# Kernel optimization log

Hardware: AMD Instinct MI355X
Metric: run time of the kernel (lower is better)

## Reference

```python
import jax, jax.numpy as jnp
import numpy as np

INPUT_DIM = 1024
HIDDEN_DIM = 1024
NUM_HEADS = 16
HEAD_DIM = HIDDEN_DIM // NUM_HEADS


def setup_inputs() -> dict:
    key = jax.random.key(0)
    ks = jax.random.split(key, 11)
    B, S = 2, 2048
    s_in = 1.0 / np.sqrt(INPUT_DIM)
    s_hid = 1.0 / np.sqrt(HIDDEN_DIM)
    return {
        "query": jax.random.normal(ks[0], (B, S, INPUT_DIM), jnp.float32),
        "key": jax.random.normal(ks[1], (B, S, INPUT_DIM), jnp.float32),
        "value": jax.random.normal(ks[2], (B, S, INPUT_DIM), jnp.float32),
        "Wq": jax.random.normal(ks[3], (INPUT_DIM, HIDDEN_DIM), jnp.float32) * s_in,
        "bq": jnp.zeros((HIDDEN_DIM,), jnp.float32),
        "Wk": jax.random.normal(ks[4], (INPUT_DIM, HEAD_DIM), jnp.float32) * s_in,
        "bk": jnp.zeros((HEAD_DIM,), jnp.float32),
        "Wv": jax.random.normal(ks[5], (INPUT_DIM, HEAD_DIM), jnp.float32) * s_in,
        "bv": jnp.zeros((HEAD_DIM,), jnp.float32),
        "Wo": jax.random.normal(ks[6], (HIDDEN_DIM, INPUT_DIM), jnp.float32) * s_hid,
        "bo": jnp.zeros((INPUT_DIM,), jnp.float32),
    }


def reference(query, key, value, Wq, bq, Wk, bk, Wv, bv, Wo, bo):
    B, S, _ = query.shape
    # projections
    q = query @ Wq + bq                       # [B,S,H*D]
    k = key @ Wk + bk                         # [B,S,D]  (single shared head)
    v = value @ Wv + bv                       # [B,S,D]
    q = q.reshape(B, S, NUM_HEADS, HEAD_DIM)  # [B,S,H,D]
    # MQA scores: shared K broadcast over query heads
    scores = jnp.einsum('bqhd,bkd->bhqk', q, k) / np.sqrt(HIDDEN_DIM)
    attn = jax.nn.softmax(scores, axis=-1)    # [B,H,Q,K]
    out = jnp.einsum('bhqk,bkd->bqhd', attn, v)  # [B,Q,H,D]
    out = out.reshape(B, S, HIDDEN_DIM)
    return out @ Wo + bo
```

## Files before the change

kernel.cpp:

```cpp
#include <hip/hip_runtime.h>


typedef unsigned int   u32;
typedef unsigned short u16;
typedef union { float4 v; float f[4]; } f4u;
typedef __attribute__((ext_vector_type(8)))  short frag16;
typedef __attribute__((ext_vector_type(4)))  float f32x4;
typedef __attribute__((ext_vector_type(16))) float f32x16;
typedef union { frag16 v; u32 w[4]; u16 e[8]; } bf8u;

static __device__ __forceinline__ u16 f2bf(float x) {
  union { float f; u32 u; } v; v.f = x;
  u32 r = v.u + 0x7fff + ((v.u >> 16) & 1);
  return (u16)(r >> 16);
}

static __device__ __forceinline__ u32 cvt_pk_bf16(float lo, float hi) {
  u32 r;
  asm("v_cvt_pk_bf16_f32 %0, %1, %2" : "=v"(r) : "v"(lo), "v"(hi));
  return r;
}

static __device__ __forceinline__ void gload_lds16(const u16* g, u16* l) {
  __builtin_amdgcn_global_load_lds(
      (const __attribute__((address_space(1))) u32*)g,
      (__attribute__((address_space(3))) u32*)l, 16, 0, 0);
}

static __device__ void tcvt_tile(const float* __restrict__ src,
                                 u16* __restrict__ dst,
                                 int C, int ldT, int rt, int ct,
                                 float (*t)[65]) {
  const int r0 = rt * 64, c0 = ct * 64;
  const int tr  = threadIdx.x >> 4;
  const int tc4 = (threadIdx.x & 15) * 4;
#pragma unroll
  for (int i = 0; i < 4; ++i) {
    f4u v; v.v = *(const float4*)(src + (size_t)(r0 + tr + i * 16) * C + c0 + tc4);
    t[tr + i * 16][tc4 + 0] = v.f[0];
    t[tr + i * 16][tc4 + 1] = v.f[1];
    t[tr + i * 16][tc4 + 2] = v.f[2];
    t[tr + i * 16][tc4 + 3] = v.f[3];
  }
  __syncthreads();
#pragma unroll
  for (int i = 0; i < 4; ++i) {
    const int oc = tr + i * 16;
    ushort4 o;
    o.x = f2bf(t[tc4 + 0][oc]);
    o.y = f2bf(t[tc4 + 1][oc]);
    o.z = f2bf(t[tc4 + 2][oc]);
    o.w = f2bf(t[tc4 + 3][oc]);
    *(ushort4*)(dst + (size_t)(c0 + oc) * ldT + r0 + tc4) = o;
  }
}

__global__ __launch_bounds__(256)
void prep_w(const float* __restrict__ Wq, const float* __restrict__ Wo,
            const float* __restrict__ Wk, const float* __restrict__ Wv,
            const float* __restrict__ query,
            u16* __restrict__ wq_t, u16* __restrict__ wo_t,
            u16* __restrict__ wk_t, u16* __restrict__ wv_t,
            u16* __restrict__ xq_bf) {
  const int bid = blockIdx.x;
  if (bid >= 544) {
    const size_t base = (size_t)(bid - 544) * 4096 + threadIdx.x * 16;
    f4u x0, x1, x2, x3;
    x0.v = *(const float4*)(query + base);
    x1.v = *(const float4*)(query + base + 4);
    x2.v = *(const float4*)(query + base + 8);
    x3.v = *(const float4*)(query + base + 12);
    bf8u t0, t1;
    t0.w[0] = cvt_pk_bf16(x0.f[0], x0.f[1]);
    t0.w[1] = cvt_pk_bf16(x0.f[2], x0.f[3]);
    t0.w[2] = cvt_pk_bf16(x1.f[0], x1.f[1]);
    t0.w[3] = cvt_pk_bf16(x1.f[2], x1.f[3]);
    t1.w[0] = cvt_pk_bf16(x2.f[0], x2.f[1]);
    t1.w[1] = cvt_pk_bf16(x2.f[2], x2.f[3]);
    t1.w[2] = cvt_pk_bf16(x3.f[0], x3.f[1]);
    t1.w[3] = cvt_pk_bf16(x3.f[2], x3.f[3]);
    *(frag16*)(xq_bf + base)     = t0.v;
    *(frag16*)(xq_bf + base + 8) = t1.v;
    return;
  }
  __shared__ float t[64][65];
  if (bid < 256)      tcvt_tile(Wq, wq_t, 1024, 1024, bid >> 4, bid & 15, t);
  else if (bid < 512) tcvt_tile(Wo, wo_t, 1024, 1024, (bid - 256) >> 4, (bid - 256) & 15, t);
  else if (bid < 528) tcvt_tile(Wk, wk_t, 64, 1024, bid - 512, 0, t);
  else                tcvt_tile(Wv, wv_t, 64, 1024, bid - 528, 0, t);
}

static __device__ void gemm128n64(const u16* __restrict__ Abf,
                                  const u16* __restrict__ Bt,
                                  const float* __restrict__ bias,
                                  void* __restrict__ Cout, int out_mode,
                                  float oscale, int row0, int col0,
                                  int N, int K, u16* As, u16* Bs) {
  const int tid  = threadIdx.x;
  const int lane = tid & 63;
  const int quad = lane >> 4, l15 = lane & 15;
  const int w = tid >> 6, wy = w >> 1, wx = w & 1;
  const int lrow = lane >> 3, lcol = (lane & 7) * 8;

  f32x4 acc[4][2];
#pragma unroll
  for (int i = 0; i < 4; ++i)
#pragma unroll
    for (int j = 0; j < 2; ++j) {
      acc[i][j][0] = 0.f; acc[i][j][1] = 0.f;
      acc[i][j][2] = 0.f; acc[i][j][3] = 0.f;
    }

  const u16* ag = Abf + (size_t)(row0 + w * 32 + lrow) * K + lcol;
  const u16* bg = Bt  + (size_t)(col0 + w * 16 + lrow) * K + lcol;
  u16* alds = As + w * 4 * 512;
  u16* blds = Bs + w * 2 * 512;

  for (int k0 = 0; k0 < K; k0 += 64) {
    __syncthreads();
#pragma unroll
    for (int i = 0; i < 4; ++i)
      gload_lds16(ag + (size_t)i * 8 * K + k0, alds + i * 512);
#pragma unroll
    for (int i = 0; i < 2; ++i)
      gload_lds16(bg + (size_t)i * 8 * K + k0, blds + i * 512);
    __syncthreads();
#pragma unroll
    for (int ks = 0; ks < 2; ++ks) {
      frag16 af[4], bfr[2];
#pragma unroll
      for (int i = 0; i < 4; ++i)
        af[i] = *(const frag16*)(&As[(wy * 64 + i * 16 + l15) * 64 + ks * 32 + quad * 8]);
#pragma unroll
      for (int j = 0; j < 2; ++j)
        bfr[j] = *(const frag16*)(&Bs[(wx * 32 + j * 16 + l15) * 64 + ks * 32 + quad * 8]);
#pragma unroll
      for (int i = 0; i < 4; ++i)
#pragma unroll
        for (int j = 0; j < 2; ++j)
          acc[i][j] = __builtin_amdgcn_mfma_f32_16x16x32_bf16(af[i], bfr[j], acc[i][j], 0, 0, 0);
    }
  }

  float bj[2];
#pragma unroll
  for (int j = 0; j < 2; ++j)
    bj[j] = bias[col0 + wx * 32 + j * 16 + l15];

#pragma unroll
  for (int i = 0; i < 4; ++i)
#pragma unroll
    for (int rr = 0; rr < 4; ++rr) {
      const size_t row = row0 + wy * 64 + i * 16 + quad * 4 + rr;
#pragma unroll
      for (int j = 0; j < 2; ++j) {
        const float v = (acc[i][j][rr] + bj[j]) * oscale;
        const int col = col0 + wx * 32 + j * 16 + l15;
        if (out_mode == 0) ((float*)Cout)[row * N + col] = v;
        else               ((u16*)Cout)[row * N + col] = f2bf(v);
      }
    }
}

#define GP 72
template <bool A_FP32>
static __device__ void gemm64(const float* __restrict__ Af32,
                              const u16* __restrict__ Abf,
                              const u16* __restrict__ Bt,
                              const float* __restrict__ bias,
                              void* __restrict__ Cout, int out_mode,
                              float oscale,
                              int row0, int col0, int N, int K, int ldT,
                              u16* As, u16* Bs) {
  const int tid  = threadIdx.x;
  const int lane = tid & 63;
  const int quad = lane >> 4, l15 = lane & 15;
  const int w = tid >> 6, wy = w >> 1, wx = w & 1;

  f32x4 acc[2][2];
#pragma unroll
  for (int i = 0; i < 2; ++i)
#pragma unroll
    for (int j = 0; j < 2; ++j) {
      acc[i][j][0] = 0.f; acc[i][j][1] = 0.f;
      acc[i][j][2] = 0.f; acc[i][j][3] = 0.f;
    }

  const int r = tid >> 2, c16 = (tid & 3) * 16;

  for (int k0 = 0; k0 < K; k0 += 64) {
    frag16 a0, a1;
    if (A_FP32) {
      const float* ap = Af32 + (size_t)(row0 + r) * K + k0 + c16;
      f4u x0, x1, x2, x3;
      x0.v = *(const float4*)(ap);
      x1.v = *(const float4*)(ap + 4);
      x2.v = *(const float4*)(ap + 8);
      x3.v = *(const float4*)(ap + 12);
      bf8u t0, t1;
      t0.w[0] = cvt_pk_bf16(x0.f[0], x0.f[1]);
      t0.w[1] = cvt_pk_bf16(x0.f[2], x0.f[3]);
      t0.w[2] = cvt_pk_bf16(x1.f[0], x1.f[1]);
      t0.w[3] = cvt_pk_bf16(x1.f[2], x1.f[3]);
      t1.w[0] = cvt_pk_bf16(x2.f[0], x2.f[1]);
      t1.w[1] = cvt_pk_bf16(x2.f[2], x2.f[3]);
      t1.w[2] = cvt_pk_bf16(x3.f[0], x3.f[1]);
      t1.w[3] = cvt_pk_bf16(x3.f[2], x3.f[3]);
      a0 = t0.v; a1 = t1.v;
    } else {
      const u16* ap = Abf + (size_t)(row0 + r) * K + k0 + c16;
      a0 = *(const frag16*)(ap);
      a1 = *(const frag16*)(ap + 8);
    }
    const u16* bp = Bt + (size_t)(col0 + r) * K + k0 + c16;
    const frag16 b0 = *(const frag16*)(bp);
    const frag16 b1 = *(const frag16*)(bp + 8);
    __syncthreads();
    *(frag16*)(&As[r * GP + c16])     = a0;
    *(frag16*)(&As[r * GP + c16 + 8]) = a1;
    *(frag16*)(&Bs[r * GP + c16])     = b0;
    *(frag16*)(&Bs[r * GP + c16 + 8]) = b1;
    __syncthreads();
#pragma unroll
    for (int ks = 0; ks < 2; ++ks) {
      frag16 af[2], bf[2];
#pragma unroll
      for (int i = 0; i < 2; ++i)
        af[i] = *(const frag16*)(&As[(wy * 32 + i * 16 + l15) * GP + ks * 32 + quad * 8]);
#pragma unroll
      for (int j = 0; j < 2; ++j)
        bf[j] = *(const frag16*)(&Bs[(wx * 32 + j * 16 + l15) * GP + ks * 32 + quad * 8]);
#pragma unroll
      for (int i = 0; i < 2; ++i)
#pragma unroll
        for (int j = 0; j < 2; ++j)
          acc[i][j] = __builtin_amdgcn_mfma_f32_16x16x32_bf16(af[i], bf[j], acc[i][j], 0, 0, 0);
    }
  }

  float bj[2];
#pragma unroll
  for (int j = 0; j < 2; ++j)
    bj[j] = bias[col0 + wx * 32 + j * 16 + l15];

#pragma unroll
  for (int i = 0; i < 2; ++i) {
#pragma unroll
    for (int rr = 0; rr < 4; ++rr) {
      const size_t row = row0 + wy * 32 + i * 16 + quad * 4 + rr;
#pragma unroll
      for (int j = 0; j < 2; ++j) {
        const float v = (acc[i][j][rr] + bj[j]) * oscale;
        const int col = col0 + wx * 32 + j * 16 + l15;
        if (out_mode == 0)      ((float*)Cout)[row * N + col] = v;
        else if (out_mode == 1) ((u16*)Cout)[row * N + col] = f2bf(v);
        else                    ((u16*)Cout)[(size_t)col * ldT + row] = f2bf(v);
      }
    }
  }
}

#define C2_SCALE 0.045084220027780106f

__global__ __launch_bounds__(256, 4)
void proj2(const float* __restrict__ key, const float* __restrict__ value,
           const u16* __restrict__ xq_bf,
           const u16* __restrict__ wq_t, const u16* __restrict__ wk_t,
           const u16* __restrict__ wv_t,
           const float* __restrict__ bq, const float* __restrict__ bk,
           const float* __restrict__ bv,
           u16* __restrict__ q_bf, u16* __restrict__ k_bf,
           u16* __restrict__ vt_bf, int M, int K) {
  __shared__ __align__(16) u16 smem[12288];
  const int bid = blockIdx.x;
  if (bid < 512)
    gemm128n64(xq_bf, wq_t, bq, q_bf, 1, C2_SCALE,
               (bid >> 4) * 128, (bid & 15) * 64, 1024, K, smem, smem + 8192);
  else if (bid < 576)
    gemm64<true>(key, nullptr, wk_t, bk, k_bf, 1, 1.0f,
                 (bid - 512) * 64, 0, 64, K, 0, smem, smem + 64 * GP);
  else
    gemm64<true>(value, nullptr, wv_t, bv, vt_bf, 2, 1.0f,
                 (bid - 576) * 64, 0, 64, K, M, smem, smem + 64 * GP);
}

__global__ __launch_bounds__(256, 4)
void out_proj(const u16* __restrict__ ao, const u16* __restrict__ wo_t,
              const float* __restrict__ bo, float* __restrict__ out,
              int M, int K) {
  __shared__ __align__(16) u16 smem[12288];
  const int bid = blockIdx.x;
  gemm128n64(ao, wo_t, bo, out, 0, 1.0f,
             (bid >> 4) * 128, (bid & 15) * 64, 1024, K, smem, smem + 8192);
}

#define APITCH 72

__global__ __launch_bounds__(256, 4)
void mqa_flash_mfma(const u16* __restrict__ Qb,
                    const u16* __restrict__ Kb,
                    const u16* __restrict__ Vt,
                    u16* __restrict__ O) {
  const int S = 2048, HID = 1024, D = 64, BS = 4096;
  __shared__ u16 Ks[64 * APITCH];
  __shared__ u16 Vs[64 * APITCH];
  __shared__ u16 Ps[64 * APITCH];
  __shared__ float red[2][64];

  const int tid  = threadIdx.x;
  const int lane = tid & 63;
  const int w    = tid >> 6;
  const int l31  = lane & 31;
  const int hh   = lane >> 5;
  const int kh   = w & 1;
  const int qh   = w >> 1;
  const int qb = blockIdx.x, h = blockIdx.y, b = blockIdx.z;

  const int sr = tid >> 3;
  const int sc = (tid & 7) * 8;

  const u16* qrow = Qb + (size_t)(b * S + qb * 64 + qh * 32 + l31) * HID + h * D;
  frag16 qf[4];
#pragma unroll
  for (int ks = 0; ks < 4; ++ks)
    qf[ks] = *(const frag16*)(qrow + ks * 16 + hh * 8);

  f32x16 zero16;
#pragma unroll
  for (int r = 0; r < 16; ++r) zero16[r] = 0.f;

  f32x16 o_acc;
#pragma unroll
  for (int r = 0; r < 16; ++r) o_acc[r] = 0.f;
  float l_lane = 0.f;

  const u16* kbase = Kb + (size_t)(b * S) * D;
  const u16* vbase = Vt + (size_t)(b * S);

  frag16 pk0 = *(const frag16*)(kbase + (size_t)sr * D + sc);
  frag16 pk1 = *(const frag16*)(kbase + (size_t)(sr + 32) * D + sc);
  frag16 pv0 = *(const frag16*)(vbase + (size_t)sr * BS + sc);
  frag16 pv1 = *(const frag16*)(vbase + (size_t)(sr + 32) * BS + sc);
  *(frag16*)(&Ks[sr * APITCH + sc])        = pk0;
  *(frag16*)(&Ks[(sr + 32) * APITCH + sc]) = pk1;
  *(frag16*)(&Vs[sr * APITCH + sc])        = pv0;
  *(frag16*)(&Vs[(sr + 32) * APITCH + sc]) = pv1;
  __syncthreads();

  for (int kc = 0; kc < S; kc += 64) {
    const int nc = (kc + 64 < S) ? kc + 64 : kc;
    pk0 = *(const frag16*)(kbase + (size_t)(nc + sr) * D + sc);
    pk1 = *(const frag16*)(kbase + (size_t)(nc + sr + 32) * D + sc);
    pv0 = *(const frag16*)(vbase + (size_t)sr * BS + nc + sc);
    pv1 = *(const frag16*)(vbase + (size_t)(sr + 32) * BS + nc + sc);

    frag16 vf[4];
#pragma unroll
    for (int ks = 0; ks < 4; ++ks)
      vf[ks] = *(const frag16*)(&Vs[(kh * 32 + l31) * APITCH + ks * 16 + hh * 8]);

    f32x16 sa;
#pragma unroll
    for (int ks = 0; ks < 4; ++ks) {
      const frag16 kf = *(const frag16*)(&Ks[(kh * 32 + l31) * APITCH + ks * 16 + hh * 8]);
      sa = __builtin_amdgcn_mfma_f32_32x32x16_bf16(kf, qf[ks], ks ? sa : zero16, 0, 0, 0);
    }

    const int qrow_l = qh * 32 + l31;
    u16* prow = &Ps[qrow_l * APITCH + kh * 32];
#pragma unroll
    for (int g = 0; g < 4; ++g) {
      const float p0 = __builtin_amdgcn_exp2f(sa[g * 4 + 0]);
      const float p1 = __builtin_amdgcn_exp2f(sa[g * 4 + 1]);
      const float p2 = __builtin_amdgcn_exp2f(sa[g * 4 + 2]);
      const float p3 = __builtin_amdgcn_exp2f(sa[g * 4 + 3]);
      l_lane += (p0 + p1) + (p2 + p3);
      uint2 pk;
      pk.x = cvt_pk_bf16(p0, p1);
      pk.y = cvt_pk_bf16(p2, p3);
      *(uint2*)(&prow[g * 8 + hh * 4]) = pk;
    }
    __syncthreads();

#pragma unroll
    for (int ks = 0; ks < 4; ++ks) {
      const frag16 pf = *(const frag16*)(&Ps[(qh * 32 + l31) * APITCH + ks * 16 + hh * 8]);
      o_acc = __builtin_amdgcn_mfma_f32_32x32x16_bf16(pf, vf[ks], o_acc, 0, 0, 0);
    }

    *(frag16*)(&Ks[sr * APITCH + sc])        = pk0;
    *(frag16*)(&Ks[(sr + 32) * APITCH + sc]) = pk1;
    *(frag16*)(&Vs[sr * APITCH + sc])        = pv0;
    *(frag16*)(&Vs[(sr + 32) * APITCH + sc]) = pv1;
    __syncthreads();
  }

  l_lane += __shfl_xor(l_lane, 32);
  __syncthreads();
  if (lane < 32) red[kh][qh * 32 + l31] = l_lane;
  __syncthreads();

#pragma unroll
  for (int r = 0; r < 16; ++r) {
    const int q_local = qh * 32 + (r & 3) + 8 * (r >> 2) + 4 * hh;
    const float li = 1.f / (red[0][q_local] + red[1][q_local]);
    u16* orow = O + (size_t)(b * S + qb * 64 + q_local) * HID + h * D;
    orow[kh * 32 + l31] = f2bf(o_acc[r] * li);
  }
}

extern "C" void kernel_launch(void* const* d_in, const int* in_sizes, int n_in,
                              void* d_out, int out_size, void* d_ws, size_t ws_size,
                              hipStream_t stream) {
  const float* query = (const float*)d_in[0];
  const float* key   = (const float*)d_in[1];
  const float* value = (const float*)d_in[2];
  const float* Wq    = (const float*)d_in[3];
  const float* bq    = (const float*)d_in[4];
  const float* Wk    = (const float*)d_in[5];
  const float* bk    = (const float*)d_in[6];
  const float* Wv    = (const float*)d_in[7];
  const float* bv    = (const float*)d_in[8];
  const float* Wo    = (const float*)d_in[9];
  const float* bo    = (const float*)d_in[10];
  float* out = (float*)d_out;

  const int B = 2, S = 2048, IN = 1024, HID = 1024, H = 16, D = 64;
  const int M = B * S;
  const size_t MB = 1024 * 1024;

  char* ws = (char*)d_ws;
  u16* q_bf  = (u16*)ws;
  u16* ao_bf = (u16*)(ws + 8 * MB);
  u16* xq_bf = ao_bf;
  u16* k_bf  = (u16*)(ws + 16 * MB);
  u16* vt_bf = (u16*)(ws + 16 * MB + 512 * 1024);
  u16* wq_t  = (u16*)(ws + 17 * MB);
  u16* wo_t  = (u16*)(ws + 19 * MB);
  u16* wk_t  = (u16*)(ws + 21 * MB);
  u16* wv_t  = (u16*)(ws + 21 * MB + 128 * 1024);

  dim3 blk(256);
  prep_w<<<dim3(1568), blk, 0, stream>>>(Wq, Wo, Wk, Wv, query,
                                         wq_t, wo_t, wk_t, wv_t, xq_bf);
  proj2<<<dim3(640), blk, 0, stream>>>(key, value, xq_bf, wq_t, wk_t, wv_t,
                                       bq, bk, bv, q_bf, k_bf, vt_bf, M, IN);
  mqa_flash_mfma<<<dim3(S / 64, H, B), blk, 0, stream>>>(q_bf, k_bf, vt_bf, ao_bf);
  out_proj<<<dim3(512), blk, 0, stream>>>(ao_bf, wo_t, bo, out, M, HID);
}
```

Before: 208.4 us.

## Give each wave its own head in MQA flash kernel, loading K/V directly

Restructures the attention kernel so each of the four waves in a block handles a different head over the same 32 query rows. Each wave computes all 64 keys of a chunk, with two score and two output accumulators. K and V fragments are read straight from global memory into registers instead of being staged through shared LDS with a software prefetch. Only a per-wave P buffer remains in LDS, which removes every block-level barrier from the main loop. In exchange it raises register pressure (launch bounds drop to 2 blocks per SIMD) and relies on cache hits for K/V, which are now re-read by each wave instead of shared once per block.

```diff
diff --git a/kernel.cpp b/kernel.cpp
--- a/kernel.cpp
+++ b/kernel.cpp
@@ -294,32 +294,26 @@
              (bid >> 4) * 128, (bid & 15) * 64, 1024, K, smem, smem + 8192);
 }
 
-#define APITCH 72
-
-__global__ __launch_bounds__(256, 4)
+#define PP 72
+
+__global__ __launch_bounds__(256, 2)
 void mqa_flash_mfma(const u16* __restrict__ Qb,
                     const u16* __restrict__ Kb,
                     const u16* __restrict__ Vt,
                     u16* __restrict__ O) {
   const int S = 2048, HID = 1024, D = 64, BS = 4096;
-  __shared__ u16 Ks[64 * APITCH];
-  __shared__ u16 Vs[64 * APITCH];
-  __shared__ u16 Ps[64 * APITCH];
-  __shared__ float red[2][64];
+  __shared__ __align__(16) u16 Ps[4][32 * PP];
+  __shared__ float lred[4][32];
 
   const int tid  = threadIdx.x;
   const int lane = tid & 63;
   const int w    = tid >> 6;
   const int l31  = lane & 31;
   const int hh   = lane >> 5;
-  const int kh   = w & 1;
-  const int qh   = w >> 1;
-  const int qb = blockIdx.x, h = blockIdx.y, b = blockIdx.z;
-
-  const int sr = tid >> 3;
-  const int sc = (tid & 7) * 8;
-
-  const u16* qrow = Qb + (size_t)(b * S + qb * 64 + qh * 32 + l31) * HID + h * D;
+  const int qb = blockIdx.x, hg = blockIdx.y, b = blockIdx.z;
+  const int h = hg * 4 + w;
+
+  const u16* qrow = Qb + (size_t)(b * S + qb * 32 + l31) * HID + h * D;
   frag16 qf[4];
 #pragma unroll
   for (int ks = 0; ks < 4; ++ks)
@@ -328,84 +322,76 @@
   f32x16 zero16;
 #pragma unroll
   for (int r = 0; r < 16; ++r) zero16[r] = 0.f;
-
-  f32x16 o_acc;
-#pragma unroll
-  for (int r = 0; r < 16; ++r) o_acc[r] = 0.f;
+  f32x16 oa0, oa1;
+#pragma unroll
+  for (int r = 0; r < 16; ++r) { oa0[r] = 0.f; oa1[r] = 0.f; }
   float l_lane = 0.f;
 
   const u16* kbase = Kb + (size_t)(b * S) * D;
   const u16* vbase = Vt + (size_t)(b * S);
-
-  frag16 pk0 = *(const frag16*)(kbase + (size_t)sr * D + sc);
-  frag16 pk1 = *(const frag16*)(kbase + (size_t)(sr + 32) * D + sc);
-  frag16 pv0 = *(const frag16*)(vbase + (size_t)sr * BS + sc);
-  frag16 pv1 = *(const frag16*)(vbase + (size_t)(sr + 32) * BS + sc);
-  *(frag16*)(&Ks[sr * APITCH + sc])        = pk0;
-  *(frag16*)(&Ks[(sr + 32) * APITCH + sc]) = pk1;
-  *(frag16*)(&Vs[sr * APITCH + sc])        = pv0;
-  *(frag16*)(&Vs[(sr + 32) * APITCH + sc]) = pv1;
-  __syncthreads();
+  u16* psw = Ps[w];
 
   for (int kc = 0; kc < S; kc += 64) {
-    const int nc = (kc + 64 < S) ? kc + 64 : kc;
-    pk0 = *(const frag16*)(kbase + (size_t)(nc + sr) * D + sc);
-    pk1 = *(const frag16*)(kbase + (size_t)(nc + sr + 32) * D + sc);
-    pv0 = *(const frag16*)(vbase + (size_t)sr * BS + nc + sc);
-    pv1 = *(const frag16*)(vbase + (size_t)(sr + 32) * BS + nc + sc);
-
-    frag16 vf[4];
+    frag16 kf0[4], kf1[4], vf0[4], vf1[4];
+#pragma unroll
+    for (int ks = 0; ks < 4; ++ks) {
+      kf0[ks] = *(const frag16*)(kbase + (size_t)(kc + l31) * D + ks * 16 + hh * 8);
+      kf1[ks] = *(const frag16*)(kbase + (size_t)(kc + 32 + l31) * D + ks * 16 + hh * 8);
+      vf0[ks] = *(const frag16*)(vbase + (size_t)l31 * BS + kc + ks * 16 + hh * 8);
+      vf1[ks] = *(const frag16*)(vbase + (size_t)(32 + l31) * BS + kc + ks * 16 + hh * 8);
+    }
+
+    f32x16 sa0, sa1;
 #pragma unroll
     for (int ks = 0; ks < 4; ++ks)
-      vf[ks] = *(const frag16*)(&Vs[(kh * 32 + l31) * APITCH + ks * 16 + hh * 8]);
-
-    f32x16 sa;
+      sa0 = __builtin_amdgcn_mfma_f32_32x32x16_bf16(kf0[ks], qf[ks], ks ? sa0 : zero16, 0, 0, 0);
+#pragma unroll
+    for (int ks = 0; ks < 4; ++ks)
+      sa1 = __builtin_amdgcn_mfma_f32_32x32x16_bf16(kf1[ks], qf[ks], ks ? sa1 : zero16, 0, 0, 0);
+
+    u16* prow = &psw[l31 * PP];
+#pragma unroll
+    for (int g = 0; g < 4; ++g) {
+      const float p0 = __builtin_amdgcn_exp2f(sa0[g * 4 + 0]);
+      const float p1 = __builtin_amdgcn_exp2f(sa0[g * 4 + 1]);
+      const float p2 = __builtin_amdgcn_exp2f(sa0[g * 4 + 2]);
+      const float p3 = __builtin_amdgcn_exp2f(sa0[g * 4 + 3]);
+      const float q0 = __builtin_amdgcn_exp2f(sa1[g * 4 + 0]);
+      const float q1 = __builtin_amdgcn_exp2f(sa1[g * 4 + 1]);
+      const float q2 = __builtin_amdgcn_exp2f(sa1[g * 4 + 2]);
+      const float q3 = __builtin_amdgcn_exp2f(sa1[g * 4 + 3]);
+      l_lane += ((p0 + p1) + (p2 + p3)) + ((q0 + q1) + (q2 + q3));
+      uint2 pk;
+      pk.x = cvt_pk_bf16(p0, p1); pk.y = cvt_pk_bf16(p2, p3);
+      *(uint2*)(&prow[g * 8 + hh * 4]) = pk;
+      uint2 qk;
+      qk.x = cvt_pk_bf16(q0, q1); qk.y = cvt_pk_bf16(q2, q3);
+      *(uint2*)(&prow[32 + g * 8 + hh * 4]) = qk;
+    }
+
 #pragma unroll
     for (int ks = 0; ks < 4; ++ks) {
-      const frag16 kf = *(const frag16*)(&Ks[(kh * 32 + l31) * APITCH + ks * 16 + hh * 8]);
-      sa = __builtin_amdgcn_mfma_f32_32x32x16_bf16(kf, qf[ks], ks ? sa : zero16, 0, 0, 0);
-    }
-
-    const int qrow_l = qh * 32 + l31;
-    u16* prow = &Ps[qrow_l * APITCH + kh * 32];
-#pragma unroll
-    for (int g = 0; g < 4; ++g) {
-      const float p0 = __builtin_amdgcn_exp2f(sa[g * 4 + 0]);
-      const float p1 = __builtin_amdgcn_exp2f(sa[g * 4 + 1]);
-      const float p2 = __builtin_amdgcn_exp2f(sa[g * 4 + 2]);
-      const float p3 = __builtin_amdgcn_exp2f(sa[g * 4 + 3]);
-      l_lane += (p0 + p1) + (p2 + p3);
-      uint2 pk;
-      pk.x = cvt_pk_bf16(p0, p1);
-      pk.y = cvt_pk_bf16(p2, p3);
-      *(uint2*)(&prow[g * 8 + hh * 4]) = pk;
-    }
-    __syncthreads();
-
-#pragma unroll
-    for (int ks = 0; ks < 4; ++ks) {
-      const frag16 pf = *(const frag16*)(&Ps[(qh * 32 + l31) * APITCH + ks * 16 + hh * 8]);
-      o_acc = __builtin_amdgcn_mfma_f32_32x32x16_bf16(pf, vf[ks], o_acc, 0, 0, 0);
-    }
-
-    *(frag16*)(&Ks[sr * APITCH + sc])        = pk0;
-    *(frag16*)(&Ks[(sr + 32) * APITCH + sc]) = pk1;
-    *(frag16*)(&Vs[sr * APITCH + sc])        = pv0;
-    *(frag16*)(&Vs[(sr + 32) * APITCH + sc]) = pv1;
-    __syncthreads();
+      const frag16 pf = *(const frag16*)(&psw[l31 * PP + ks * 16 + hh * 8]);
+      oa0 = __builtin_amdgcn_mfma_f32_32x32x16_bf16(pf, vf0[ks], oa0, 0, 0, 0);
+      oa1 = __builtin_amdgcn_mfma_f32_32x32x16_bf16(pf, vf1[ks], oa1, 0, 0, 0);
+    }
   }
 
   l_lane += __shfl_xor(l_lane, 32);
-  __syncthreads();
-  if (lane < 32) red[kh][qh * 32 + l31] = l_lane;
-  __syncthreads();
-
-#pragma unroll
-  for (int r = 0; r < 16; ++r) {
-    const int q_local = qh * 32 + (r & 3) + 8 * (r >> 2) + 4 * hh;
-    const float li = 1.f / (red[0][q_local] + red[1][q_local]);
-    u16* orow = O + (size_t)(b * S + qb * 64 + q_local) * HID + h * D;
-    orow[kh * 32 + l31] = f2bf(o_acc[r] * li);
+  lred[w][l31] = l_lane;
+
+#pragma unroll
+  for (int g2 = 0; g2 < 4; ++g2) {
+    const f32x4 lv = *(const f32x4*)(&lred[w][g2 * 8 + hh * 4]);
+#pragma unroll
+    for (int m = 0; m < 4; ++m) {
+      const int r = g2 * 4 + m;
+      const int q_local = g2 * 8 + hh * 4 + m;
+      const float li = 1.f / lv[m];
+      u16* orow = O + (size_t)(b * S + qb * 32 + q_local) * HID + h * D;
+      orow[l31]      = f2bf(oa0[r] * li);
+      orow[32 + l31] = f2bf(oa1[r] * li);
+    }
   }
 }
 
@@ -445,6 +431,6 @@
                                          wq_t, wo_t, wk_t, wv_t, xq_bf);
   proj2<<<dim3(640), blk, 0, stream>>>(key, value, xq_bf, wq_t, wk_t, wv_t,
                                        bq, bk, bv, q_bf, k_bf, vt_bf, M, IN);
-  mqa_flash_mfma<<<dim3(S / 64, H, B), blk, 0, stream>>>(q_bf, k_bf, vt_bf, ao_bf);
+  mqa_flash_mfma<<<dim3(S / 32, H / 4, B), blk, 0, stream>>>(q_bf, k_bf, vt_bf, ao_bf);
   out_proj<<<dim3(512), blk, 0, stream>>>(ao_bf, wo_t, bo, out, M, HID);
 }
```

After: 275.5 us. 1.32x slower.
